# Performance work log

Measured on AMD Instinct MI355X. Metric: run time of the kernel, lower is better.

## Reference

```python
import jax, jax.numpy as jnp
import numpy as np

SHAPES = ((496, 432), (248, 216), (124, 108))
NS = (40000, 20000, 8000)
T = 32
B = 4
EPS = 1e-3


def _bn(x, g, b, m, v):
    return (x - m) * (g / jnp.sqrt(v + EPS)) + b


def _vfe_scale(voxels, num_pts, w1, p1, w2, p2):
    # voxels: (N, T, 4); num_pts: (N,)
    Tp = voxels.shape[1]
    n = num_pts.astype(voxels.dtype)[:, None, None]
    m3 = voxels[:, :, :3].sum(axis=1, keepdims=True) / n
    m2 = voxels[:, :, :2].sum(axis=1, keepdims=True) / n
    feat = jnp.concatenate([voxels[:, :, :4], voxels[:, :, :3] - m3, voxels[:, :, :2] - m2], axis=-1)  # (N,T,9)
    mask = (jnp.arange(Tp)[None, :] < num_pts[:, None]).astype(voxels.dtype)[:, :, None]
    x = feat
    for w, (g, b_, rm, rv) in ((w1, p1), (w2, p2)):
        h = jax.nn.relu(_bn(jnp.einsum('ntc,cd->ntd', x, w), g, b_, rm, rv))  # (N,T,64)
        gmax = h.max(axis=1, keepdims=True)  # global max includes padded rows, as in torch source
        x = jnp.concatenate([h, jnp.broadcast_to(gmax, h.shape)], axis=-1) * mask  # (N,T,128)
    return x.max(axis=1)[:, :64]  # (N,64)


def _scatter_bev(vf, coords, h, w, batch_size):
    b = coords[:, 0]
    y = jnp.clip(coords[:, 2], 0, h - 1)
    x = jnp.clip(coords[:, 3], 0, w - 1)
    grid = jnp.zeros((batch_size, vf.shape[1], h, w), vf.dtype)
    return grid.at[b, :, y, x].set(vf)


def _fusion(x, w, g, b, m, v):
    y = jax.lax.conv_general_dilated(x, w, (1, 1), ((1, 1), (1, 1)),
                                     dimension_numbers=('NCHW', 'OIHW', 'NCHW'))
    y = _bn(y, g[None, :, None, None], b[None, :, None, None], m[None, :, None, None], v[None, :, None, None])
    return jax.nn.relu(y)


def setup_inputs() -> dict:
    key = jax.random.key(0)
    ks = jax.random.split(key, 32)
    inp = {}
    for s in range(3):
        h, w = SHAPES[s]
        inp[f'voxels_{s}'] = jax.random.normal(ks[s], (NS[s], T, 4), dtype=jnp.float32)
        inp[f'num_pts_{s}'] = jax.random.randint(ks[3 + s], (NS[s],), 1, T + 1, dtype=jnp.int32)
        b = jax.random.randint(ks[6 + s], (NS[s],), 0, B, dtype=jnp.int32)
        z = jnp.zeros((NS[s],), jnp.int32)
        y = jax.random.randint(ks[9 + s], (NS[s],), 0, h, dtype=jnp.int32)
        x = jax.random.randint(ks[12 + s], (NS[s],), 0, w, dtype=jnp.int32)
        inp[f'coords_{s}'] = jnp.stack([b, z, y, x], axis=1)
    # VFE params (stacked across the 3 scales; identical shapes per scale)
    inp['w1'] = jax.random.normal(ks[15], (3, 9, 64), dtype=jnp.float32) * 0.1
    inp['g1'] = jnp.ones((3, 64), jnp.float32) + 0.1 * jax.random.normal(ks[16], (3, 64))
    inp['b1'] = 0.05 * jax.random.normal(ks[17], (3, 64))
    inp['rm1'] = 0.05 * jax.random.normal(ks[18], (3, 64))
    inp['rv1'] = 0.5 + jnp.abs(jax.random.normal(ks[19], (3, 64)))
    inp['w2'] = jax.random.normal(ks[20], (3, 128, 64), dtype=jnp.float32) * 0.05
    inp['g2'] = jnp.ones((3, 64), jnp.float32) + 0.1 * jax.random.normal(ks[21], (3, 64))
    inp['b2'] = 0.05 * jax.random.normal(ks[22], (3, 64))
    inp['rm2'] = 0.05 * jax.random.normal(ks[23], (3, 64))
    inp['rv2'] = 0.5 + jnp.abs(jax.random.normal(ks[24], (3, 64)))
    # Fusion convs (2): Conv2d(128,64,3) + BN
    inp['fw'] = jax.random.normal(ks[25], (2, 64, 128, 3, 3), dtype=jnp.float32) * 0.03
    inp['fg'] = jnp.ones((2, 64), jnp.float32) + 0.1 * jax.random.normal(ks[26], (2, 64))
    inp['fb'] = 0.05 * jax.random.normal(ks[27], (2, 64))
    inp['fm'] = 0.05 * jax.random.normal(ks[28], (2, 64))
    inp['fv'] = 0.5 + jnp.abs(jax.random.normal(ks[29], (2, 64)))
    inp['batch_size'] = B
    return inp


def reference(voxels_0, voxels_1, voxels_2,
              w1, g1, b1, rm1, rv1, w2, g2, b2, rm2, rv2,
              fw, fg, fb, fm, fv,
              num_pts_0, num_pts_1, num_pts_2,
              coords_0, coords_1, coords_2, batch_size):
    voxels = (voxels_0, voxels_1, voxels_2)
    num_pts = (num_pts_0, num_pts_1, num_pts_2)
    coords = (coords_0, coords_1, coords_2)
    sf = []
    for s in range(3):
        vf = _vfe_scale(voxels[s], num_pts[s],
                        w1[s], (g1[s], b1[s], rm1[s], rv1[s]),
                        w2[s], (g2[s], b2[s], rm2[s], rv2[s]))
        h, w = SHAPES[s]
        sf.append(_scatter_bev(vf, coords[s], h, w, batch_size))
    # bottom-up fusion: scale2 -> scale1 -> scale0
    up = jax.image.resize(sf[2], sf[1].shape[:2] + SHAPES[1], method='bilinear')
    fused_1 = _fusion(jnp.concatenate([sf[1], up], axis=1), fw[1], fg[1], fb[1], fm[1], fv[1])
    up = jax.image.resize(fused_1, fused_1.shape[:2] + SHAPES[0], method='bilinear')
    fused_0 = _fusion(jnp.concatenate([sf[0], up], axis=1), fw[0], fg[0], fb[0], fm[0], fv[0])
    return fused_0  # spatial_features_2d: (B, 64, 496, 432)
```

## Files before the change

kernel.cpp:

```cpp
#include <hip/hip_runtime.h>

typedef unsigned short u16;
typedef short bf16x8 __attribute__((ext_vector_type(8)));
typedef float f32x4 __attribute__((ext_vector_type(4)));

#define EPSV 1e-3f

__device__ __forceinline__ float bf2f(u16 u) {
  union { unsigned int i; float f; } x; x.i = ((unsigned int)u) << 16; return x.f;
}
__device__ __forceinline__ u16 f2bf(float f) {
  union { float f; unsigned int i; } x; x.f = f;
  unsigned int r = x.i + 0x7fffu + ((x.i >> 16) & 1u);
  return (u16)(r >> 16);
}

#define WAVE_FENCE() do { __builtin_amdgcn_s_waitcnt(0); __builtin_amdgcn_wave_barrier(); } while (0)

__global__ void twt_kernel(const float* __restrict__ fw, u16* __restrict__ fwT) {
  int i = blockIdx.x * blockDim.x + threadIdx.x;
  if (i >= 2 * 4 * 9 * 64 * 32) return;
  int ciq = i & 31;
  int r = i >> 5;
  int co = r & 63; r >>= 6;
  int tap = r % 9; r /= 9;
  int qk = r & 3;
  int set = r >> 2;
  int ci = qk * 32 + ciq;
  fwT[i] = f2bf(fw[(((set * 64 + co) * 128 + ci) * 9) + tap]);
}

__global__ __launch_bounds__(256, 2) void vfe_mfma_kernel(
    const float* __restrict__ vox, const int* __restrict__ npts,
    const float* __restrict__ w1, const float* __restrict__ g1, const float* __restrict__ b1,
    const float* __restrict__ rm1, const float* __restrict__ rv1,
    const float* __restrict__ w2, const float* __restrict__ g2, const float* __restrict__ b2,
    const float* __restrict__ rm2, const float* __restrict__ rv2,
    float* __restrict__ vf, int N)
{
  struct PerWave {
    u16 X[32 * 72];
    u16 F[32 * 40];
    u16 G[64];
  };
  __shared__ __align__(16) union {
    struct { u16 W1T[64 * 40]; u16 W2T[64 * 136]; } w;
    PerWave r[4];
  } lds;

  const int tid = threadIdx.x;
  const int lane = tid & 63;
  const int wv = tid >> 6;
  const int m16 = lane & 15;
  const int q = lane >> 4;

  for (int i = tid; i < 64 * 40; i += 256) {
    int c = i / 40, k = i % 40;
    lds.w.W1T[i] = f2bf(k < 9 ? w1[k * 64 + c] : 0.f);
  }
  for (int i = tid; i < 64 * 136; i += 256) {
    int c = i / 136, j = i % 136;
    lds.w.W2T[i] = f2bf(j < 128 ? w2[j * 64 + c] : 0.f);
  }
  __syncthreads();

  bf16x8 bW1[4], bLo[4][2], bHi[4][2];
  float sc1[4], sh1[4], sc2[4], sh2[4];
#pragma unroll
  for (int nf = 0; nf < 4; ++nf) {
    int c = nf * 16 + m16;
    bW1[nf] = *(const bf16x8*)&lds.w.W1T[c * 40 + q * 8];
#pragma unroll
    for (int ks = 0; ks < 2; ++ks) {
      bLo[nf][ks] = *(const bf16x8*)&lds.w.W2T[c * 136 + ks * 32 + q * 8];
      bHi[nf][ks] = *(const bf16x8*)&lds.w.W2T[c * 136 + 64 + ks * 32 + q * 8];
    }
    float s1 = g1[c] * rsqrtf(rv1[c] + EPSV);
    sc1[nf] = s1; sh1[nf] = b1[c] - rm1[c] * s1;
    float s2 = g2[c] * rsqrtf(rv2[c] + EPSV);
    sc2[nf] = s2; sh2[nf] = b2[c] - rm2[c] * s2;
  }
  __syncthreads();

  u16* X = lds.r[wv].X;
  u16* F = lds.r[wv].F;
  u16* G = lds.r[wv].G;
  for (int i = lane; i < 640; i += 64) ((unsigned int*)F)[i] = 0u;

  const int wgid = blockIdx.x * 4 + wv;
  const int wstride = gridDim.x * 4;

  for (int v = wgid; v < N; v += wstride) {
    const int n = npts[v];
    float px = 0.f, py = 0.f, pz = 0.f, pw = 0.f;
    if (lane < 32) {
      float4 u = *(const float4*)(vox + ((size_t)v * 32 + lane) * 4);
      px = u.x; py = u.y; pz = u.z; pw = u.w;
    }
    float sx = px, sy = py, sz = pz;
#pragma unroll
    for (int off = 32; off >= 1; off >>= 1) {
      sx += __shfl_xor(sx, off);
      sy += __shfl_xor(sy, off);
      sz += __shfl_xor(sz, off);
    }
    float nf_ = (float)n;
    float mx = sx / nf_, my = sy / nf_, mz = sz / nf_;
    if (lane < 32) {
      float dx = px - mx, dy = py - my, dz = pz - mz;
      bf16x8 r0, r1;
      r0[0] = (short)f2bf(px); r0[1] = (short)f2bf(py);
      r0[2] = (short)f2bf(pz); r0[3] = (short)f2bf(pw);
      r0[4] = (short)f2bf(dx); r0[5] = (short)f2bf(dy);
      r0[6] = (short)f2bf(dz); r0[7] = (short)f2bf(dx);
      r1 = (bf16x8){0, 0, 0, 0, 0, 0, 0, 0};
      r1[0] = (short)f2bf(dy);
      *(bf16x8*)&F[lane * 40 + 0] = r0;
      *(bf16x8*)&F[lane * 40 + 8] = r1;
    }
    WAVE_FENCE();

    bf16x8 a1[2];
    a1[0] = *(const bf16x8*)&F[m16 * 40 + q * 8];
    a1[1] = *(const bf16x8*)&F[(16 + m16) * 40 + q * 8];
    f32x4 acc1[2][4];
#pragma unroll
    for (int mf = 0; mf < 2; ++mf)
#pragma unroll
      for (int nf = 0; nf < 4; ++nf) {
        acc1[mf][nf] = (f32x4){0.f, 0.f, 0.f, 0.f};
        acc1[mf][nf] = __builtin_amdgcn_mfma_f32_16x16x32_bf16(a1[mf], bW1[nf], acc1[mf][nf], 0, 0, 0);
      }

    float gmx[4] = {0.f, 0.f, 0.f, 0.f};
#pragma unroll
    for (int mf = 0; mf < 2; ++mf)
#pragma unroll
      for (int nf = 0; nf < 4; ++nf)
#pragma unroll
        for (int r = 0; r < 4; ++r) {
          float h = fmaxf(acc1[mf][nf][r] * sc1[nf] + sh1[nf], 0.f);
          gmx[nf] = fmaxf(gmx[nf], h);
          int t = mf * 16 + q * 4 + r;
          X[t * 72 + nf * 16 + m16] = f2bf(h);
        }
#pragma unroll
    for (int nf = 0; nf < 4; ++nf) {
      gmx[nf] = fmaxf(gmx[nf], __shfl_xor(gmx[nf], 16));
      gmx[nf] = fmaxf(gmx[nf], __shfl_xor(gmx[nf], 32));
    }
    if (q == 0) {
#pragma unroll
      for (int nf = 0; nf < 4; ++nf) G[nf * 16 + m16] = f2bf(gmx[nf]);
    }
    WAVE_FENCE();

    f32x4 ga[4];
#pragma unroll
    for (int nf = 0; nf < 4; ++nf) ga[nf] = (f32x4){0.f, 0.f, 0.f, 0.f};
#pragma unroll
    for (int ks = 0; ks < 2; ++ks) {
      bf16x8 ag = (bf16x8){0, 0, 0, 0, 0, 0, 0, 0};
      if (m16 == 0) ag = *(const bf16x8*)&G[ks * 32 + q * 8];
#pragma unroll
      for (int nf = 0; nf < 4; ++nf)
        ga[nf] = __builtin_amdgcn_mfma_f32_16x16x32_bf16(ag, bHi[nf][ks], ga[nf], 0, 0, 0);
    }
    float gt[4];
#pragma unroll
    for (int nf = 0; nf < 4; ++nf) {
      float s = ga[nf][0] + ga[nf][1] + ga[nf][2] + ga[nf][3];
      s += __shfl_xor(s, 16);
      s += __shfl_xor(s, 32);
      gt[nf] = s;
    }

    f32x4 acc2[2][4];
#pragma unroll
    for (int mf = 0; mf < 2; ++mf)
#pragma unroll
      for (int nf = 0; nf < 4; ++nf)
        acc2[mf][nf] = (f32x4){gt[nf], gt[nf], gt[nf], gt[nf]};
#pragma unroll
    for (int ks = 0; ks < 2; ++ks) {
      bf16x8 a2[2];
      a2[0] = *(const bf16x8*)&X[m16 * 72 + ks * 32 + q * 8];
      a2[1] = *(const bf16x8*)&X[(16 + m16) * 72 + ks * 32 + q * 8];
#pragma unroll
      for (int mf = 0; mf < 2; ++mf)
#pragma unroll
        for (int nf = 0; nf < 4; ++nf)
          acc2[mf][nf] = __builtin_amdgcn_mfma_f32_16x16x32_bf16(a2[mf], bLo[nf][ks], acc2[mf][nf], 0, 0, 0);
    }

    float vm[4] = {0.f, 0.f, 0.f, 0.f};
#pragma unroll
    for (int mf = 0; mf < 2; ++mf)
#pragma unroll
      for (int nf = 0; nf < 4; ++nf)
#pragma unroll
        for (int r = 0; r < 4; ++r) {
          int t = mf * 16 + q * 4 + r;
          float h2 = fmaxf(acc2[mf][nf][r] * sc2[nf] + sh2[nf], 0.f);
          if (t < n) vm[nf] = fmaxf(vm[nf], h2);
        }
#pragma unroll
    for (int nf = 0; nf < 4; ++nf) {
      vm[nf] = fmaxf(vm[nf], __shfl_xor(vm[nf], 16));
      vm[nf] = fmaxf(vm[nf], __shfl_xor(vm[nf], 32));
    }
    float outv = (q == 0) ? vm[0] : (q == 1) ? vm[1] : (q == 2) ? vm[2] : vm[3];
    vf[(size_t)v * 64 + q * 16 + m16] = outv;
    __builtin_amdgcn_wave_barrier();
  }
}

__global__ void winner_kernel(const int* __restrict__ coords, int* __restrict__ win,
                              int N, int H, int W) {
  int v = blockIdx.x * blockDim.x + threadIdx.x;
  if (v >= N) return;
  int b = coords[v * 4 + 0];
  int y = min(max(coords[v * 4 + 2], 0), H - 1);
  int x = min(max(coords[v * 4 + 3], 0), W - 1);
  atomicMax(&win[(b * H + y) * W + x], v);
}

__global__ void fill_kernel(const int* __restrict__ win, const float* __restrict__ vf,
                            u16* __restrict__ dst, int cells, size_t ps, int planar) {
  int i = blockIdx.x * blockDim.x + threadIdx.x;
  if (i >= cells * 8) return;
  int cell = i >> 3, c8 = (i & 7) * 8;
  int wv = win[cell];
  bf16x8 o = (bf16x8){0, 0, 0, 0, 0, 0, 0, 0};
  if (wv >= 0) {
    const float* p = vf + (size_t)wv * 64 + c8;
    float4 v0 = *(const float4*)p;
    float4 v1 = *(const float4*)(p + 4);
    o[0] = (short)f2bf(v0.x); o[1] = (short)f2bf(v0.y);
    o[2] = (short)f2bf(v0.z); o[3] = (short)f2bf(v0.w);
    o[4] = (short)f2bf(v1.x); o[5] = (short)f2bf(v1.y);
    o[6] = (short)f2bf(v1.z); o[7] = (short)f2bf(v1.w);
  }
  u16* d = planar ? (dst + (size_t)(c8 >> 5) * ps + (size_t)cell * 32 + (c8 & 31))
                  : (dst + (size_t)cell * 64 + c8);
  *(bf16x8*)d = o;
}

__global__ void upsample_kernel(const u16* __restrict__ src, u16* __restrict__ dst,
                                int Hc, int Wc, size_t ps, int total8) {
  int i = blockIdx.x * blockDim.x + threadIdx.x;
  if (i >= total8) return;
  int c8 = (i & 7) * 8;
  int px = i >> 3;
  int W2 = Wc * 2, H2 = Hc * 2;
  int x = px % W2; int t = px / W2; int y = t % H2; int n = t / H2;
  int ky = y >> 1, kx = x >> 1;
  int ya, yb, xa, xb; float wya, wxa;
  if ((y & 1) == 0) { ya = ky > 0 ? ky - 1 : 0; yb = ky; wya = 0.25f; }
  else              { ya = ky; yb = (ky + 1 < Hc) ? ky + 1 : Hc - 1; wya = 0.75f; }
  if ((x & 1) == 0) { xa = kx > 0 ? kx - 1 : 0; xb = kx; wxa = 0.25f; }
  else              { xa = kx; xb = (kx + 1 < Wc) ? kx + 1 : Wc - 1; wxa = 0.75f; }
  float wyb = 1.f - wya, wxb = 1.f - wxa;
  const u16* sp = src + c8;
  bf16x8 vaa = *(const bf16x8*)&sp[((size_t)(n * Hc + ya) * Wc + xa) * 64];
  bf16x8 vab = *(const bf16x8*)&sp[((size_t)(n * Hc + ya) * Wc + xb) * 64];
  bf16x8 vba = *(const bf16x8*)&sp[((size_t)(n * Hc + yb) * Wc + xa) * 64];
  bf16x8 vbb = *(const bf16x8*)&sp[((size_t)(n * Hc + yb) * Wc + xb) * 64];
  bf16x8 o;
#pragma unroll
  for (int j = 0; j < 8; ++j) {
    float v = wya * (wxa * bf2f((u16)vaa[j]) + wxb * bf2f((u16)vab[j])) +
              wyb * (wxa * bf2f((u16)vba[j]) + wxb * bf2f((u16)vbb[j]));
    o[j] = (short)f2bf(v);
  }
  *(bf16x8*)&dst[(size_t)(2 + (c8 >> 5)) * ps + (size_t)px * 32 + (c8 & 31)] = o;
}

template<int H, int W, bool NCHW_OUT>
__global__ __launch_bounds__(256, 2) void conv_kernel(
    const u16* __restrict__ in, const u16* __restrict__ wT,
    const float* __restrict__ fg, const float* __restrict__ fb,
    const float* __restrict__ fm, const float* __restrict__ fv,
    void* __restrict__ outv)
{
  constexpr int XT = 32, YT = 16;
  constexpr int XTILES = (W + XT - 1) / XT;
  constexpr int YTILES = (H + YT - 1) / YT;
  constexpr int HC = XT + 2;
  constexpr int NPX = (YT + 2) * HC;
  const size_t PS = (size_t)4 * H * W * 32;
  __shared__ __align__(16) union {
    struct { char A[(NPX / 2) * 128]; char B[9 * 4096]; } s;
    float T[4 * 64 * 33];
  } lds;

  const int tid = threadIdx.x;
  const int lane = tid & 63;
  const int wv = tid >> 6;
  const int m16 = lane & 15;
  const int q = lane >> 4;

  int bid = blockIdx.x;
  const int xt = bid % XTILES; bid /= XTILES;
  const int yt = bid % YTILES;
  const int n = bid / YTILES;
  const int x0 = xt * XT, y0 = yt * YT;

  int lin[8];
#pragma unroll
  for (int mf = 0; mf < 8; ++mf)
    lin[mf] = (wv * 4 + (mf >> 1)) * HC + ((mf & 1) << 4) + m16;

  const int bbase = ((m16 >> 1) << 7) + (((((m16 & 1) << 2) + q) ^ (m16 >> 1)) << 4);

  f32x4 acc[8][4];
#pragma unroll
  for (int mf = 0; mf < 8; ++mf)
#pragma unroll
    for (int nf = 0; nf < 4; ++nf)
      acc[mf][nf] = (f32x4){0.f, 0.f, 0.f, 0.f};

  for (int qk = 0; qk < 4; ++qk) {
    if (qk) __syncthreads();
    {
      const u16* inq = in + (size_t)qk * PS;
#pragma unroll
      for (int it = 0; it < 10; ++it) {
        int c = tid + it * 256;
        if (c < NPX * 4) {
          int p = c >> 2, s = c & 3;
          int r = p / HC, xx = p - r * HC;
          int gy = y0 - 1 + r, gx = x0 - 1 + xx;
          uint4 v = make_uint4(0, 0, 0, 0);
          if (gy >= 0 && gy < H && gx >= 0 && gx < W)
            v = *(const uint4*)(inq + ((size_t)((n * H + gy) * W + gx)) * 32 + s * 8);
          int slot = (((p & 1) << 2) + s) ^ ((p >> 1) & 7);
          *(uint4*)(lds.s.A + ((p >> 1) << 7) + (slot << 4)) = v;
        }
      }
      const u16* wq = wT + qk * (9 * 64 * 32);
#pragma unroll
      for (int it = 0; it < 9; ++it) {
        int c = tid + it * 256;
        int tap = c >> 8, c2 = c & 255;
        int co = c2 >> 2, s = c2 & 3;
        uint4 v = *(const uint4*)(wq + tap * 2048 + co * 32 + s * 8);
        int slot = (((co & 1) << 2) + s) ^ ((co >> 1) & 7);
        *(uint4*)(lds.s.B + (tap << 12) + ((co >> 1) << 7) + (slot << 4)) = v;
      }
    }
    __syncthreads();

#pragma unroll
    for (int tap = 0; tap < 9; ++tap) {
      const int ky = tap / 3, kx = tap - ky * 3;
      const int tapofs = ky * HC + kx;
      bf16x8 b[4];
#pragma unroll
      for (int nf = 0; nf < 4; ++nf)
        b[nf] = *(const bf16x8*)(lds.s.B + (tap << 12) + (nf << 10) + bbase);
      bf16x8 a[8];
#pragma unroll
      for (int mf = 0; mf < 8; ++mf) {
        int hp = lin[mf] + tapofs;
        int slot = (((hp & 1) << 2) + q) ^ ((hp >> 1) & 7);
        a[mf] = *(const bf16x8*)(lds.s.A + ((hp >> 1) << 7) + (slot << 4));
      }
#pragma unroll
      for (int mf = 0; mf < 8; ++mf)
#pragma unroll
        for (int nf = 0; nf < 4; ++nf)
          acc[mf][nf] = __builtin_amdgcn_mfma_f32_16x16x32_bf16(a[mf], b[nf], acc[mf][nf], 0, 0, 0);
    }
  }

  float sc[4], sh[4];
#pragma unroll
  for (int nf = 0; nf < 4; ++nf) {
    int co = nf * 16 + m16;
    float s = fg[co] * rsqrtf(fv[co] + EPSV);
    sc[nf] = s;
    sh[nf] = fb[co] - fm[co] * s;
  }

  if (!NCHW_OUT) {
    u16* out = (u16*)outv;
#pragma unroll
    for (int mf = 0; mf < 8; ++mf) {
      int y = y0 + wv * 4 + (mf >> 1);
      if (y < H) {
#pragma unroll
        for (int nf = 0; nf < 4; ++nf)
#pragma unroll
          for (int r = 0; r < 4; ++r) {
            int px = ((mf & 1) << 4) + q * 4 + r;
            int x = x0 + px;
            if (x < W) {
              int co = nf * 16 + m16;
              float v = fmaxf(acc[mf][nf][r] * sc[nf] + sh[nf], 0.f);
              out[((size_t)(n * H + y) * W + x) * 64 + co] = f2bf(v);
            }
          }
      }
    }
  } else {
    __syncthreads();
    float* out = (float*)outv;
    float* T = &lds.T[wv * 64 * 33];
#pragma unroll
    for (int rr = 0; rr < 4; ++rr) {
      int y = y0 + wv * 4 + rr;
#pragma unroll
      for (int xc = 0; xc < 2; ++xc)
#pragma unroll
        for (int nf = 0; nf < 4; ++nf)
#pragma unroll
          for (int r = 0; r < 4; ++r) {
            int px = (xc << 4) + q * 4 + r;
            int co = nf * 16 + m16;
            T[co * 33 + px] = fmaxf(acc[rr * 2 + xc][nf][r] * sc[nf] + sh[nf], 0.f);
          }
      WAVE_FENCE();
      const int px = lane & 31, co2 = lane >> 5;
      int x = x0 + px;
      if (y < H) {
#pragma unroll 4
        for (int it = 0; it < 32; ++it) {
          int co = it * 2 + co2;
          float v = T[co * 33 + px];
          if (x < W) out[((size_t)(n * 64 + co) * H + y) * W + x] = v;
        }
      }
      WAVE_FENCE();
    }
  }
}

extern "C" void kernel_launch(void* const* d_in, const int* in_sizes, int n_in,
                              void* d_out, int out_size, void* d_ws, size_t ws_size,
                              hipStream_t stream) {
  int I_vox[3], I_np[3], I_co[3];
  int I_w1, I_g1, I_b1, I_rm1, I_rv1, I_w2, I_g2, I_b2, I_rm2, I_rv2;
  int I_fw, I_fg, I_fb, I_fm, I_fv;
  if (in_sizes[1] == 40000) {
    I_vox[0] = 0; I_np[0] = 1; I_co[0] = 2;
    I_vox[1] = 3; I_np[1] = 4; I_co[1] = 5;
    I_vox[2] = 6; I_np[2] = 7; I_co[2] = 8;
    I_w1 = 9; I_g1 = 10; I_b1 = 11; I_rm1 = 12; I_rv1 = 13;
    I_w2 = 14; I_g2 = 15; I_b2 = 16; I_rm2 = 17; I_rv2 = 18;
    I_fw = 19; I_fg = 20; I_fb = 21; I_fm = 22; I_fv = 23;
  } else {
    I_vox[0] = 0; I_vox[1] = 1; I_vox[2] = 2;
    I_w1 = 3; I_g1 = 4; I_b1 = 5; I_rm1 = 6; I_rv1 = 7;
    I_w2 = 8; I_g2 = 9; I_b2 = 10; I_rm2 = 11; I_rv2 = 12;
    I_fw = 13; I_fg = 14; I_fb = 15; I_fm = 16; I_fv = 17;
    I_np[0] = 18; I_np[1] = 19; I_np[2] = 20;
    I_co[0] = 21; I_co[1] = 22; I_co[2] = 23;
  }

  const int HS[3] = {496, 248, 124};
  const int WS[3] = {432, 216, 108};
  int Nv[3];
  for (int s = 0; s < 3; ++s) Nv[s] = in_sizes[I_np[s]];

  char* wsp = (char*)d_ws;
  size_t off = 0;
  auto take = [&](size_t bytes) -> void* {
    void* p = wsp + off;
    off = (off + bytes + 255) & ~(size_t)255;
    return p;
  };
  float* vf[3]; int* win[3];
  for (int s = 0; s < 3; ++s) vf[s] = (float*)take((size_t)Nv[s] * 64 * 4);
  int cells[3];
  for (int s = 0; s < 3; ++s) {
    cells[s] = 4 * HS[s] * WS[s];
    win[s] = (int*)take((size_t)cells[s] * 4);
  }
  u16* buf0 = (u16*)take((size_t)cells[0] * 128 * 2);
  u16* buf1 = (u16*)take((size_t)cells[1] * 128 * 2);
  u16* g2b  = (u16*)take((size_t)cells[2] * 64 * 2);
  u16* fus1 = (u16*)take((size_t)cells[1] * 64 * 2);
  u16* fwT  = (u16*)take((size_t)2 * 4 * 9 * 64 * 32 * 2);

  const float* W1 = (const float*)d_in[I_w1];
  const float* G1 = (const float*)d_in[I_g1];
  const float* B1 = (const float*)d_in[I_b1];
  const float* RM1 = (const float*)d_in[I_rm1];
  const float* RV1 = (const float*)d_in[I_rv1];
  const float* W2 = (const float*)d_in[I_w2];
  const float* G2 = (const float*)d_in[I_g2];
  const float* B2 = (const float*)d_in[I_b2];
  const float* RM2 = (const float*)d_in[I_rm2];
  const float* RV2 = (const float*)d_in[I_rv2];
  const float* FW = (const float*)d_in[I_fw];
  const float* FG = (const float*)d_in[I_fg];
  const float* FB = (const float*)d_in[I_fb];
  const float* FM = (const float*)d_in[I_fm];
  const float* FV = (const float*)d_in[I_fv];

  for (int s = 0; s < 3; ++s)
    hipMemsetAsync(win[s], 0xFF, (size_t)cells[s] * 4, stream);

  twt_kernel<<<(2 * 4 * 9 * 64 * 32 + 255) / 256, 256, 0, stream>>>(FW, fwT);

  for (int s = 0; s < 3; ++s) {
    int blocks = (Nv[s] + 3) / 4;
    if (blocks > 1024) blocks = 1024;
    vfe_mfma_kernel<<<blocks, 256, 0, stream>>>(
        (const float*)d_in[I_vox[s]], (const int*)d_in[I_np[s]],
        W1 + s * 9 * 64, G1 + s * 64, B1 + s * 64, RM1 + s * 64, RV1 + s * 64,
        W2 + s * 128 * 64, G2 + s * 64, B2 + s * 64, RM2 + s * 64, RV2 + s * 64,
        vf[s], Nv[s]);
  }
  for (int s = 0; s < 3; ++s) {
    winner_kernel<<<(Nv[s] + 255) / 256, 256, 0, stream>>>(
        (const int*)d_in[I_co[s]], win[s], Nv[s], HS[s], WS[s]);
  }
  const size_t ps0 = (size_t)cells[0] * 32;
  const size_t ps1 = (size_t)cells[1] * 32;
  fill_kernel<<<(cells[0] * 8 + 255) / 256, 256, 0, stream>>>(win[0], vf[0], buf0, cells[0], ps0, 1);
  fill_kernel<<<(cells[1] * 8 + 255) / 256, 256, 0, stream>>>(win[1], vf[1], buf1, cells[1], ps1, 1);
  fill_kernel<<<(cells[2] * 8 + 255) / 256, 256, 0, stream>>>(win[2], vf[2], g2b, cells[2], 0, 0);

  {
    int total8 = cells[1] * 8;
    upsample_kernel<<<(total8 + 255) / 256, 256, 0, stream>>>(g2b, buf1, 124, 108, ps1, total8);
  }
  conv_kernel<248, 216, false><<<4 * ((248 + 15) / 16) * 7, 256, 0, stream>>>(
      buf1, fwT + 4 * 9 * 64 * 32, FG + 64, FB + 64, FM + 64, FV + 64, fus1);
  {
    int total8 = cells[0] * 8;
    upsample_kernel<<<(total8 + 255) / 256, 256, 0, stream>>>(fus1, buf0, 248, 216, ps0, total8);
  }
  conv_kernel<496, 432, true><<<4 * (496 / 16) * 14, 256, 0, stream>>>(
      buf0, fwT, FG, FB, FM, FV, (float*)d_out);
}
```

Before: 764.3 us.

## Halve conv tile height, stream per-tap weights through double-buffered LDS

The conv kernel's spatial tile shrinks from 32x16 to 32x8, which halves the accumulators per wave and raises launch bounds to 3 blocks per SM. The full 9-tap weight block in LDS is replaced by a two-slot buffer that is filled one tap at a time, with the next tap prefetched from global memory during the current tap's MFMAs. The NCHW epilogue transposes 32 channels at a time to fit the smaller LDS. In exchange, each tap now ends in a block-wide barrier, and halo overhead per output pixel rises, as do global weight reloads per block.

```diff
diff --git a/kernel.cpp b/kernel.cpp
--- a/kernel.cpp
+++ b/kernel.cpp
@@ -277,21 +277,21 @@
 }
 
 template<int H, int W, bool NCHW_OUT>
-__global__ __launch_bounds__(256, 2) void conv_kernel(
+__global__ __launch_bounds__(256, 3) void conv_kernel(
     const u16* __restrict__ in, const u16* __restrict__ wT,
     const float* __restrict__ fg, const float* __restrict__ fb,
     const float* __restrict__ fm, const float* __restrict__ fv,
     void* __restrict__ outv)
 {
-  constexpr int XT = 32, YT = 16;
+  constexpr int XT = 32, YT = 8;
   constexpr int XTILES = (W + XT - 1) / XT;
-  constexpr int YTILES = (H + YT - 1) / YT;
+  constexpr int YTILES = H / YT;
   constexpr int HC = XT + 2;
   constexpr int NPX = (YT + 2) * HC;
   const size_t PS = (size_t)4 * H * W * 32;
   __shared__ __align__(16) union {
-    struct { char A[(NPX / 2) * 128]; char B[9 * 4096]; } s;
-    float T[4 * 64 * 33];
+    struct { char A[(NPX / 2) * 128]; char B[2][4096]; } s;
+    float T[4 * 32 * 33];
   } lds;
 
   const int tid = threadIdx.x;
@@ -306,26 +306,31 @@
   const int n = bid / YTILES;
   const int x0 = xt * XT, y0 = yt * YT;
 
-  int lin[8];
-#pragma unroll
-  for (int mf = 0; mf < 8; ++mf)
-    lin[mf] = (wv * 4 + (mf >> 1)) * HC + ((mf & 1) << 4) + m16;
-
-  const int bbase = ((m16 >> 1) << 7) + (((((m16 & 1) << 2) + q) ^ (m16 >> 1)) << 4);
-
-  f32x4 acc[8][4];
-#pragma unroll
-  for (int mf = 0; mf < 8; ++mf)
+  int lin[4];
+#pragma unroll
+  for (int mf = 0; mf < 4; ++mf)
+    lin[mf] = (2 * wv + (mf >> 1)) * HC + ((mf & 1) << 4) + m16;
+
+  const int bbase = ((m16 >> 1) << 7) + (((((m16 & 1) << 2) + q) ^ ((m16 >> 1) & 7)) << 4);
+
+  f32x4 acc[4][4];
+#pragma unroll
+  for (int mf = 0; mf < 4; ++mf)
 #pragma unroll
     for (int nf = 0; nf < 4; ++nf)
       acc[mf][nf] = (f32x4){0.f, 0.f, 0.f, 0.f};
 
+  const int bco = tid >> 2, bs = tid & 3;
+  const int bslot = ((((bco & 1) << 2) + bs) ^ ((bco >> 1) & 7));
+  const int bldst = ((bco >> 1) << 7) + (bslot << 4);
+  const int bgsrc = bco * 32 + bs * 8;
+
   for (int qk = 0; qk < 4; ++qk) {
-    if (qk) __syncthreads();
+    const u16* inq = in + (size_t)qk * PS;
+    const u16* wq = wT + qk * (9 * 64 * 32);
     {
-      const u16* inq = in + (size_t)qk * PS;
-#pragma unroll
-      for (int it = 0; it < 10; ++it) {
+#pragma unroll
+      for (int it = 0; it < 6; ++it) {
         int c = tid + it * 256;
         if (c < NPX * 4) {
           int p = c >> 2, s = c & 3;
@@ -338,39 +343,34 @@
           *(uint4*)(lds.s.A + ((p >> 1) << 7) + (slot << 4)) = v;
         }
       }
-      const u16* wq = wT + qk * (9 * 64 * 32);
-#pragma unroll
-      for (int it = 0; it < 9; ++it) {
-        int c = tid + it * 256;
-        int tap = c >> 8, c2 = c & 255;
-        int co = c2 >> 2, s = c2 & 3;
-        uint4 v = *(const uint4*)(wq + tap * 2048 + co * 32 + s * 8);
-        int slot = (((co & 1) << 2) + s) ^ ((co >> 1) & 7);
-        *(uint4*)(lds.s.B + (tap << 12) + ((co >> 1) << 7) + (slot << 4)) = v;
-      }
+      uint4 v = *(const uint4*)(wq + bgsrc);
+      *(uint4*)(lds.s.B[0] + bldst) = v;
     }
     __syncthreads();
 
 #pragma unroll
     for (int tap = 0; tap < 9; ++tap) {
-      const int ky = tap / 3, kx = tap - ky * 3;
-      const int tapofs = ky * HC + kx;
-      bf16x8 b[4];
+      uint4 bv;
+      if (tap < 8) bv = *(const uint4*)(wq + (tap + 1) * 2048 + bgsrc);
+      const int tapofs = (tap / 3) * HC + (tap % 3);
+      const char* Bb = lds.s.B[tap & 1];
+      bf16x8 b[4], a[4];
 #pragma unroll
       for (int nf = 0; nf < 4; ++nf)
-        b[nf] = *(const bf16x8*)(lds.s.B + (tap << 12) + (nf << 10) + bbase);
-      bf16x8 a[8];
-#pragma unroll
-      for (int mf = 0; mf < 8; ++mf) {
+        b[nf] = *(const bf16x8*)(Bb + (nf << 10) + bbase);
+#pragma unroll
+      for (int mf = 0; mf < 4; ++mf) {
         int hp = lin[mf] + tapofs;
         int slot = (((hp & 1) << 2) + q) ^ ((hp >> 1) & 7);
         a[mf] = *(const bf16x8*)(lds.s.A + ((hp >> 1) << 7) + (slot << 4));
       }
 #pragma unroll
-      for (int mf = 0; mf < 8; ++mf)
+      for (int mf = 0; mf < 4; ++mf)
 #pragma unroll
         for (int nf = 0; nf < 4; ++nf)
           acc[mf][nf] = __builtin_amdgcn_mfma_f32_16x16x32_bf16(a[mf], b[nf], acc[mf][nf], 0, 0, 0);
+      if (tap < 8) *(uint4*)(lds.s.B[(tap + 1) & 1] + bldst) = bv;
+      __syncthreads();
     }
   }
 
@@ -386,52 +386,56 @@
   if (!NCHW_OUT) {
     u16* out = (u16*)outv;
 #pragma unroll
-    for (int mf = 0; mf < 8; ++mf) {
-      int y = y0 + wv * 4 + (mf >> 1);
-      if (y < H) {
-#pragma unroll
-        for (int nf = 0; nf < 4; ++nf)
-#pragma unroll
-          for (int r = 0; r < 4; ++r) {
-            int px = ((mf & 1) << 4) + q * 4 + r;
-            int x = x0 + px;
-            if (x < W) {
-              int co = nf * 16 + m16;
-              float v = fmaxf(acc[mf][nf][r] * sc[nf] + sh[nf], 0.f);
-              out[((size_t)(n * H + y) * W + x) * 64 + co] = f2bf(v);
-            }
+    for (int mf = 0; mf < 4; ++mf) {
+      int y = y0 + wv * 2 + (mf >> 1);
+#pragma unroll
+      for (int nf = 0; nf < 4; ++nf)
+#pragma unroll
+        for (int r = 0; r < 4; ++r) {
+          int px = ((mf & 1) << 4) + q * 4 + r;
+          int x = x0 + px;
+          if (x < W) {
+            int co = nf * 16 + m16;
+            float v = fmaxf(acc[mf][nf][r] * sc[nf] + sh[nf], 0.f);
+            out[((size_t)(n * H + y) * W + x) * 64 + co] = f2bf(v);
           }
-      }
+        }
     }
   } else {
     __syncthreads();
     float* out = (float*)outv;
-    float* T = &lds.T[wv * 64 * 33];
-#pragma unroll
-    for (int rr = 0; rr < 4; ++rr) {
-      int y = y0 + wv * 4 + rr;
-#pragma unroll
-      for (int xc = 0; xc < 2; ++xc)
-#pragma unroll
-        for (int nf = 0; nf < 4; ++nf)
-#pragma unroll
-          for (int r = 0; r < 4; ++r) {
-            int px = (xc << 4) + q * 4 + r;
-            int co = nf * 16 + m16;
-            T[co * 33 + px] = fmaxf(acc[rr * 2 + xc][nf][r] * sc[nf] + sh[nf], 0.f);
+    float* T = &lds.T[wv * 32 * 33];
+#pragma unroll
+    for (int rr = 0; rr < 2; ++rr) {
+      int y = y0 + wv * 2 + rr;
+#pragma unroll
+      for (int half = 0; half < 2; ++half) {
+#pragma unroll
+        for (int nfh = 0; nfh < 2; ++nfh) {
+          int nf = half * 2 + nfh;
+#pragma unroll
+          for (int xc = 0; xc < 2; ++xc) {
+            int mf = rr * 2 + xc;
+#pragma unroll
+            for (int r = 0; r < 4; ++r) {
+              int px = (xc << 4) + q * 4 + r;
+              int col = nfh * 16 + m16;
+              T[col * 33 + px] = fmaxf(acc[mf][nf][r] * sc[nf] + sh[nf], 0.f);
+            }
           }
-      WAVE_FENCE();
-      const int px = lane & 31, co2 = lane >> 5;
-      int x = x0 + px;
-      if (y < H) {
+        }
+        WAVE_FENCE();
+        const int px = lane & 31, co2 = lane >> 5;
+        int x = x0 + px;
 #pragma unroll 4
-        for (int it = 0; it < 32; ++it) {
-          int co = it * 2 + co2;
-          float v = T[co * 33 + px];
+        for (int it = 0; it < 16; ++it) {
+          int col = it * 2 + co2;
+          int co = half * 32 + col;
+          float v = T[col * 33 + px];
           if (x < W) out[((size_t)(n * 64 + co) * H + y) * W + x] = v;
         }
+        WAVE_FENCE();
       }
-      WAVE_FENCE();
     }
   }
 }
@@ -527,12 +531,12 @@
     int total8 = cells[1] * 8;
     upsample_kernel<<<(total8 + 255) / 256, 256, 0, stream>>>(g2b, buf1, 124, 108, ps1, total8);
   }
-  conv_kernel<248, 216, false><<<4 * ((248 + 15) / 16) * 7, 256, 0, stream>>>(
+  conv_kernel<248, 216, false><<<4 * (248 / 8) * 7, 256, 0, stream>>>(
       buf1, fwT + 4 * 9 * 64 * 32, FG + 64, FB + 64, FM + 64, FV + 64, fus1);
   {
     int total8 = cells[0] * 8;
     upsample_kernel<<<(total8 + 255) / 256, 256, 0, stream>>>(fus1, buf0, 248, 216, ps0, total8);
   }
-  conv_kernel<496, 432, true><<<4 * (496 / 16) * 14, 256, 0, stream>>>(
+  conv_kernel<496, 432, true><<<4 * (496 / 8) * 14, 256, 0, stream>>>(
       buf0, fwT, FG, FB, FM, FV, (float*)d_out);
 }
```

Measured after the change: 765.0 us. About the same (+0.1%).
